# Kernel tuning notes

Hardware: AMD Instinct MI355X
Metric: run time of the kernel (lower is better)

## Reference

```python
import jax, jax.numpy as jnp
import numpy as np

T, B, E, H = 1024, 8, 1024, 16
HD = E // H                       # 64
SCALE = float(HD * 1) ** -0.5     # scaling_factor = 1


def setup_inputs() -> dict:
    key = jax.random.key(0)
    ks = jax.random.split(key, 7)
    s = 0.02
    return {
        "query": jax.random.normal(ks[0], (T, B, E), jnp.float32),
        "key_padding_mask": jax.random.bernoulli(ks[1], 0.1, (B, T)),
        "attn_bias": jax.random.normal(ks[2], (1, H, T, T), jnp.float32) * 0.1,
        "wq": jax.random.normal(ks[3], (1, E, E), jnp.float32) * s,
        "wk": jax.random.normal(ks[4], (1, E, E), jnp.float32) * s,
        "wv": jax.random.normal(ks[5], (1, E, E), jnp.float32) * s,
        "wo": jax.random.normal(ks[6], (1, E, E), jnp.float32) * s,
    }


def _group_linear(x, w):
    # x: (T, B, nb*din), w: (nb, din, dout) -> (T, B, nb*dout). nb=1 here.
    t, b, _ = x.shape
    nb, din, dout = w.shape
    y = jnp.einsum('xnd,nde->xne', x.reshape(t * b, nb, din), w)
    return y.reshape(t, b, nb * dout)


def reference(query, key_padding_mask, attn_bias, wq, wk, wv, wo):
    q = _group_linear(query, wq) * SCALE
    k = _group_linear(query, wk)
    v = _group_linear(query, wv)

    # (T, B, E) -> (B*H, T, HD), matching torch view+transpose
    def split_heads(x):
        return x.reshape(T, B * H, HD).transpose(1, 0, 2)

    q, k, v = split_heads(q), split_heads(k), split_heads(v)

    scores = jnp.einsum('bth,bsh->bts', q, k).reshape(B, H, T, T)
    scores = scores + attn_bias
    scores = jnp.where(key_padding_mask[:, None, None, :], -jnp.inf, scores)
    probs = jax.nn.softmax(scores.astype(jnp.float32), axis=-1).astype(query.dtype)

    vh = v.reshape(B, H, T, HD)  # (B*H,T,HD) -> (B,H,S,HD)
    attn = jnp.einsum('bhts,bhsd->tbhd', probs, vh).reshape(T, B, H * HD)
    return _group_linear(attn, wo)
```

## Files before the change

kernel.cpp:

```cpp
#include <hip/hip_runtime.h>


typedef __bf16 bf16x8 __attribute__((ext_vector_type(8)));
typedef float f32x4 __attribute__((ext_vector_type(4)));

#define LOG2E 1.4426950408889634f
#define QSCALE 0.18033688011112042f

static __device__ __forceinline__ unsigned short f2bf_rn(float f) {
  union { float f; unsigned u; } x;
  x.f = f;
  unsigned r = (x.u + 0x7fffu + ((x.u >> 16) & 1u)) >> 16;
  return (unsigned short)r;
}
static __device__ __forceinline__ unsigned short f2bf(float f) {
  union { float f; unsigned u; } x;
  x.f = f;
  return (unsigned short)((x.u + 0x8000u) >> 16);
}

static __device__ __forceinline__ void async_cp16(const void* g, void* l) {
  __builtin_amdgcn_global_load_lds((__attribute__((address_space(1))) void*)g,
                                   (__attribute__((address_space(3))) void*)l,
                                   16, 0, 0);
}

__global__ void k_cvt(const float* __restrict__ src, unsigned short* __restrict__ dst) {
  const int idx = blockIdx.x * 256 + threadIdx.x;
  const float4 f = ((const float4*)src)[idx];
  unsigned lo = (unsigned)f2bf_rn(f.x) | ((unsigned)f2bf_rn(f.y) << 16);
  unsigned hi = (unsigned)f2bf_rn(f.z) | ((unsigned)f2bf_rn(f.w) << 16);
  uint2 v; v.x = lo; v.y = hi;
  *(uint2*)(dst + (size_t)idx * 4) = v;
}

__global__ void k_mask(const int* __restrict__ mask, float* __restrict__ Mfg) {
  const int i = blockIdx.x * 256 + threadIdx.x;
  Mfg[i] = mask[i] ? -1e30f : 0.f;
}

__global__ void k_transw(const float* __restrict__ src, unsigned short* __restrict__ dst) {
  __shared__ float tile[32][33];
  const int bx = blockIdx.x << 5;
  const int by = blockIdx.y << 5;
  const int tx = threadIdx.x, ty = threadIdx.y;
#pragma unroll
  for (int i = 0; i < 32; i += 8)
    tile[ty + i][tx] = src[(size_t)(by + ty + i) * 1024 + bx + tx];
  __syncthreads();
#pragma unroll
  for (int i = 0; i < 32; i += 8)
    dst[(size_t)(bx + ty + i) * 1024 + by + tx] = f2bf_rn(tile[tx][ty + i]);
}

__global__ __launch_bounds__(256, 2) void k_biasT(const float* __restrict__ bias,
                                                  unsigned short* __restrict__ B2) {
  __shared__ unsigned short tile[128 * 132];
  const int tid = threadIdx.x;
  const int ss = blockIdx.x, tt = blockIdx.y, h = blockIdx.z;
  const float* src = bias + ((long)h * 1024 + tt * 128) * 1024 + ss * 128;
#pragma unroll
  for (int c = 0; c < 16; ++c) {
    int flat = c * 256 + tid;
    int row = flat >> 5, col = (flat & 31) << 2;
    float4 v = *(const float4*)(src + (long)row * 1024 + col);
    unsigned short* t4 = &tile[row * 132 + col];
    t4[0] = f2bf_rn(v.x * LOG2E); t4[1] = f2bf_rn(v.y * LOG2E);
    t4[2] = f2bf_rn(v.z * LOG2E); t4[3] = f2bf_rn(v.w * LOG2E);
  }
  __syncthreads();
  const int wid = tid >> 6, lane = tid & 63, lanelo = lane & 15, quad = lane >> 4;
  unsigned short outv[64];
#pragma unroll
  for (int mi = 0; mi < 2; ++mi)
#pragma unroll
    for (int nj = 0; nj < 8; ++nj)
#pragma unroll
      for (int r = 0; r < 4; ++r)
        outv[mi * 32 + nj * 4 + r] =
            tile[(wid * 32 + mi * 16 + quad * 4 + r) * 132 + nj * 16 + lanelo];
  unsigned short* dst = B2 + ((((long)(h * 8 + tt) * 8 + ss) * 256 + tid) << 6);
#pragma unroll
  for (int i = 0; i < 8; ++i) ((uint4*)dst)[i] = ((const uint4*)outv)[i];
}

static __device__ __forceinline__ void gemm_tile_128x128(
    const unsigned short* __restrict__ A, const unsigned short* __restrict__ Bt,
    int K, long m0, long n0,
    unsigned short* As, unsigned short* Bs, f32x4 acc[4][4]) {
  const int tid = threadIdx.x;
  const int wid = tid >> 6;
  const int lane = tid & 63;
  const int lanelo = lane & 15;
  const int quad = lane >> 4;
  const int wm = (wid >> 1) << 6;
  const int wn = (wid & 1) << 6;
  const int srow = tid >> 2;
  const int scol = (tid & 3) << 3;

  for (int k0 = 0; k0 < K; k0 += 32) {
    __syncthreads();
    {
      const unsigned short* ga0 = A + (m0 + srow) * K + k0 + scol;
      const unsigned short* ga1 = A + (m0 + srow + 64) * K + k0 + scol;
      const unsigned short* gb0 = Bt + (n0 + srow) * K + k0 + scol;
      const unsigned short* gb1 = Bt + (n0 + srow + 64) * K + k0 + scol;
      char* la = (char*)As + wid * 1024;
      char* lb = (char*)Bs + wid * 1024;
      async_cp16(ga0, la);
      async_cp16(ga1, la + 4096);
      async_cp16(gb0, lb);
      async_cp16(gb1, lb + 4096);
    }
    __syncthreads();
    bf16x8 a[4], b[4];
#pragma unroll
    for (int i = 0; i < 4; ++i) {
      a[i] = *(const bf16x8*)(As + (wm + i * 16 + lanelo) * 32 + quad * 8);
      b[i] = *(const bf16x8*)(Bs + (wn + i * 16 + lanelo) * 32 + quad * 8);
    }
#pragma unroll
    for (int i = 0; i < 4; ++i)
#pragma unroll
      for (int j = 0; j < 4; ++j)
        acc[i][j] = __builtin_amdgcn_mfma_f32_16x16x32_bf16(a[i], b[j], acc[i][j], 0, 0, 0);
  }
}

__global__ __launch_bounds__(256, 2) void k_gemm_qkv(
    const unsigned short* __restrict__ A, const unsigned short* __restrict__ Bt,
    unsigned short* __restrict__ Qh, unsigned short* __restrict__ Kh,
    unsigned short* __restrict__ Vt) {
  __shared__ unsigned short smem[9216];
  unsigned short* As = smem;
  unsigned short* Bs = smem + 4096;
  f32x4 acc[4][4];
  const f32x4 z4 = {0.f, 0.f, 0.f, 0.f};
#pragma unroll
  for (int i = 0; i < 4; ++i)
#pragma unroll
    for (int j = 0; j < 4; ++j) acc[i][j] = z4;

  const long m0 = (long)blockIdx.y * 128;
  const long n0 = (long)blockIdx.x * 128;
  gemm_tile_128x128(A, Bt, 1024, m0, n0, As, Bs, acc);

  const int tid = threadIdx.x;
  const int wid = tid >> 6;
  const int lane = tid & 63;
  const int lanelo = lane & 15;
  const int quad = lane >> 4;
  const int wm = (wid >> 1) << 6;
  const int wn = (wid & 1) << 6;
  const int which = (int)(blockIdx.x >> 3);

  if (which == 2) {
    unsigned short* Vt_s = smem;
    const long t0g = m0 >> 3;
#pragma unroll
    for (int half = 0; half < 2; ++half) {
      __syncthreads();
      if ((wid & 1) == half) {
#pragma unroll
        for (int mi = 0; mi < 4; ++mi)
#pragma unroll
          for (int nj = 0; nj < 4; ++nj)
#pragma unroll
            for (int r = 0; r < 4; ++r)
              Vt_s[(wm + mi * 16 + quad * 4 + r) * 72 + nj * 16 + lanelo] =
                  f2bf(acc[mi][nj][r]);
      }
      __syncthreads();
      const int h = (((int)(n0 & 1023)) >> 6) + half;
#pragma unroll
      for (int pp = 0; pp < 2; ++pp) {
        int p = tid + pp * 256;
        int b = p >> 6, d = p & 63;
        long off = ((long)(b * 16 + h)) << 16;
        __attribute__((aligned(16))) unsigned short vals[16];
#pragma unroll
        for (int t = 0; t < 16; ++t) vals[t] = Vt_s[(t * 8 + b) * 72 + d];
        uint4* dst = (uint4*)(Vt + off + (long)d * 1024 + t0g);
        dst[0] = ((const uint4*)vals)[0];
        dst[1] = ((const uint4*)vals)[1];
      }
    }
  } else {
#pragma unroll
    for (int mi = 0; mi < 4; ++mi)
#pragma unroll
      for (int nj = 0; nj < 4; ++nj)
#pragma unroll
        for (int r = 0; r < 4; ++r) {
          int m = (int)m0 + wm + mi * 16 + quad * 4 + r;
          int n = (int)n0 + wn + nj * 16 + lanelo;
          float v = acc[mi][nj][r];
          int t = m >> 3, b = m & 7;
          int e = n & 1023, h = e >> 6, d = e & 63;
          long off = ((long)(b * 16 + h)) << 16;
          if (which == 0)
            Qh[off + t * 64 + d] = f2bf(v * QSCALE);
          else
            Kh[off + t * 64 + d] = f2bf(v);
        }
  }
}

__global__ __launch_bounds__(512, 4) void k_attn(
    const unsigned short* __restrict__ Qh, const unsigned short* __restrict__ Kh,
    const unsigned short* __restrict__ Vt, const unsigned short* __restrict__ B2,
    const float* __restrict__ Mfg, unsigned short* __restrict__ A2) {
  __shared__ unsigned short Ks[128 * 72];
  __shared__ unsigned short Vs[64 * 136];
  __shared__ unsigned short Ps[128 * 72];

  const int tid = threadIdx.x;
  const int wid = tid >> 6;
  const int lane = tid & 63;
  const int lanelo = lane & 15;
  const int quad = lane >> 4;
  const int bh = blockIdx.x;
  const int b = bh >> 4, h = bh & 15;
  const int tt = blockIdx.y;
  const int t0 = tt * 128;
  const long head = (long)bh << 16;

  bf16x8 aq[2];
#pragma unroll
  for (int ks = 0; ks < 2; ++ks)
    aq[ks] = *(const bf16x8*)(Qh + head +
                              (long)(t0 + wid * 16 + lanelo) * 64 +
                              ks * 32 + quad * 8);

  const f32x4 z4 = {0.f, 0.f, 0.f, 0.f};
  f32x4 Oacc[4];
#pragma unroll
  for (int dj = 0; dj < 4; ++dj) Oacc[dj] = z4;
  float mrow[4], lrow[4];
#pragma unroll
  for (int r = 0; r < 4; ++r) { mrow[r] = -1e30f; lrow[r] = 0.f; }

  const long biasbase = (((long)(h * 8 + tt) * 8) * 256 + (wid >> 1) * 64 + lane) * 64 +
                        (wid & 1) * 32;

  for (int s0 = 0; s0 < 1024; s0 += 128) {
    bf16x8 bfr[4];
    {
      const bf16x8* bp8 = (const bf16x8*)(B2 + biasbase + ((long)(s0 >> 7) * 256 << 6));
#pragma unroll
      for (int i = 0; i < 4; ++i) bfr[i] = bp8[i];
    }
    float madd[8];
#pragma unroll
    for (int nj = 0; nj < 8; ++nj)
      madd[nj] = Mfg[(long)b * 1024 + s0 + nj * 16 + lanelo];

    __syncthreads();
#pragma unroll
    for (int c = 0; c < 2; ++c) {
      int flat = c * 4096 + tid * 8;
      int row = flat >> 6, col = flat & 63;
      uint4 v = *(const uint4*)(Kh + head + (long)(s0 + row) * 64 + col);
      *(uint4*)&Ks[row * 72 + col] = v;
    }
#pragma unroll
    for (int c = 0; c < 2; ++c) {
      int flat = c * 4096 + tid * 8;
      int row = flat >> 7, col = flat & 127;
      uint4 v = *(const uint4*)(Vt + head + (long)row * 1024 + s0 + col);
      *(uint4*)&Vs[row * 136 + col] = v;
    }
    __syncthreads();

    f32x4 S[8];
#pragma unroll
    for (int nj = 0; nj < 8; ++nj)
#pragma unroll
      for (int r = 0; r < 4; ++r)
        S[nj][r] = (float)bfr[nj >> 1][(nj & 1) * 4 + r] + madd[nj];

#pragma unroll
    for (int ks = 0; ks < 2; ++ks) {
      bf16x8 bk[8];
#pragma unroll
      for (int nj = 0; nj < 8; ++nj)
        bk[nj] = *(const bf16x8*)(Ks + (nj * 16 + lanelo) * 72 + ks * 32 + quad * 8);
#pragma unroll
      for (int nj = 0; nj < 8; ++nj)
        S[nj] = __builtin_amdgcn_mfma_f32_16x16x32_bf16(aq[ks], bk[nj], S[nj], 0, 0, 0);
    }

#pragma unroll
    for (int r = 0; r < 4; ++r) {
      float mx = S[0][r];
#pragma unroll
      for (int nj = 1; nj < 8; ++nj) mx = fmaxf(mx, S[nj][r]);
      mx = fmaxf(mx, __shfl_xor(mx, 1, 16));
      mx = fmaxf(mx, __shfl_xor(mx, 2, 16));
      mx = fmaxf(mx, __shfl_xor(mx, 4, 16));
      mx = fmaxf(mx, __shfl_xor(mx, 8, 16));
      float mold = mrow[r];
      float mnew = fmaxf(mold, mx);
      float al = exp2f(mold - mnew);
      mrow[r] = mnew;
      float rs = 0.f;
#pragma unroll
      for (int nj = 0; nj < 8; ++nj) {
        float p = exp2f(S[nj][r] - mnew);
        S[nj][r] = p;
        rs += p;
      }
      rs += __shfl_xor(rs, 1, 16);
      rs += __shfl_xor(rs, 2, 16);
      rs += __shfl_xor(rs, 4, 16);
      rs += __shfl_xor(rs, 8, 16);
      lrow[r] = lrow[r] * al + rs;
#pragma unroll
      for (int dj = 0; dj < 4; ++dj) Oacc[dj][r] *= al;
    }

#pragma unroll
    for (int half = 0; half < 2; ++half) {
#pragma unroll
      for (int njl = 0; njl < 4; ++njl)
#pragma unroll
        for (int r = 0; r < 4; ++r)
          Ps[(wid * 16 + quad * 4 + r) * 72 + njl * 16 + lanelo] =
              f2bf(S[half * 4 + njl][r]);
#pragma unroll
      for (int ks2 = 0; ks2 < 2; ++ks2) {
        const int ks = half * 2 + ks2;
        bf16x8 ap, bv[4];
        ap = *(const bf16x8*)(Ps + (wid * 16 + lanelo) * 72 + ks2 * 32 + quad * 8);
#pragma unroll
        for (int dj = 0; dj < 4; ++dj)
          bv[dj] = *(const bf16x8*)(Vs + (dj * 16 + lanelo) * 136 + ks * 32 + quad * 8);
#pragma unroll
        for (int dj = 0; dj < 4; ++dj)
          Oacc[dj] = __builtin_amdgcn_mfma_f32_16x16x32_bf16(ap, bv[dj], Oacc[dj], 0, 0, 0);
      }
    }
  }

#pragma unroll
  for (int r = 0; r < 4; ++r) {
    float rinv = __builtin_amdgcn_rcpf(lrow[r]);
    int t = t0 + wid * 16 + quad * 4 + r;
#pragma unroll
    for (int dj = 0; dj < 4; ++dj) {
      int d = dj * 16 + lanelo;
      A2[(long)(t * 8 + b) * 1024 + h * 64 + d] = f2bf(Oacc[dj][r] * rinv);
    }
  }
}

__global__ __launch_bounds__(256, 2) void k_gemm_out(
    const unsigned short* __restrict__ A, const unsigned short* __restrict__ Bt,
    float* __restrict__ out) {
  __shared__ unsigned short As[128 * 32];
  __shared__ unsigned short Bs[128 * 32];
  f32x4 acc[4][4];
  const f32x4 z4 = {0.f, 0.f, 0.f, 0.f};
#pragma unroll
  for (int i = 0; i < 4; ++i)
#pragma unroll
    for (int j = 0; j < 4; ++j) acc[i][j] = z4;

  const long m0 = (long)blockIdx.y * 128;
  const long n0 = (long)blockIdx.x * 128;
  gemm_tile_128x128(A, Bt, 1024, m0, n0, As, Bs, acc);

  const int tid = threadIdx.x;
  const int wid = tid >> 6;
  const int lane = tid & 63;
  const int lanelo = lane & 15;
  const int quad = lane >> 4;
  const int wm = (wid >> 1) << 6;
  const int wn = (wid & 1) << 6;
#pragma unroll
  for (int mi = 0; mi < 4; ++mi)
#pragma unroll
    for (int nj = 0; nj < 4; ++nj)
#pragma unroll
      for (int r = 0; r < 4; ++r) {
        long m = m0 + wm + mi * 16 + quad * 4 + r;
        long n = n0 + wn + nj * 16 + lanelo;
        out[m * 1024 + n] = acc[mi][nj][r];
      }
}

extern "C" void kernel_launch(void* const* d_in, const int* in_sizes, int n_in,
                              void* d_out, int out_size, void* d_ws, size_t ws_size,
                              hipStream_t stream) {
  const float* query = (const float*)d_in[0];
  const int* mask = (const int*)d_in[1];
  const float* bias = (const float*)d_in[2];
  const float* wq = (const float*)d_in[3];
  const float* wk = (const float*)d_in[4];
  const float* wv = (const float*)d_in[5];
  const float* wo = (const float*)d_in[6];
  float* out = (float*)d_out;

  char* ws = (char*)d_ws;
  const size_t MB = 1024 * 1024;
  unsigned short* Abuf  = (unsigned short*)(ws);
  unsigned short* WqkvT = (unsigned short*)(ws + 16 * MB);
  unsigned short* WoT   = (unsigned short*)(ws + 22 * MB);
  unsigned short* Qh    = (unsigned short*)(ws + 24 * MB);
  unsigned short* Kh    = (unsigned short*)(ws + 40 * MB);
  unsigned short* Vt    = (unsigned short*)(ws + 56 * MB);
  unsigned short* A2    = (unsigned short*)(ws + 72 * MB);
  unsigned short* B2    = (unsigned short*)(ws + 88 * MB);
  float*          Mfg   = (float*)(ws + 120 * MB);

  k_cvt<<<dim3(8192), dim3(256), 0, stream>>>(query, Abuf);
  k_mask<<<dim3(32), dim3(256), 0, stream>>>(mask, Mfg);
  dim3 tb(32, 8);
  k_transw<<<dim3(32, 32), tb, 0, stream>>>(wq, WqkvT);
  k_transw<<<dim3(32, 32), tb, 0, stream>>>(wk, WqkvT + 1024 * 1024);
  k_transw<<<dim3(32, 32), tb, 0, stream>>>(wv, WqkvT + 2 * 1024 * 1024);
  k_transw<<<dim3(32, 32), tb, 0, stream>>>(wo, WoT);
  k_biasT<<<dim3(8, 8, 16), dim3(256), 0, stream>>>(bias, B2);
  k_gemm_qkv<<<dim3(24, 64), dim3(256), 0, stream>>>(Abuf, WqkvT, Qh, Kh, Vt);
  k_attn<<<dim3(128, 8), dim3(512), 0, stream>>>(Qh, Kh, Vt, B2, Mfg, A2);
  k_gemm_out<<<dim3(8, 64), dim3(256), 0, stream>>>(A2, WoT, out);
}
```

Baseline: 381.8 us.

## Prefetch next K/V tile and bias into registers during attention compute

Software-pipelines the flash-attention loop. The next iteration's K and V tiles are loaded into registers and stored to LDS at the top of the following iteration, and the next bias and mask values are fetched right after the QK MFMAs. The goal is to hide global memory latency behind compute instead of stalling at each tile load. In exchange, register use goes up, which could lower occupancy.

```diff
diff --git a/kernel.cpp b/kernel.cpp
--- a/kernel.cpp
+++ b/kernel.cpp
@@ -225,6 +225,13 @@
   const int t0 = tt * 128;
   const long head = (long)bh << 16;
 
+  const int krow = tid >> 3, kcol = (tid & 7) << 3;
+  const int vrow = tid >> 4, vcol = (tid & 15) << 3;
+  const unsigned short* kg = Kh + head + (long)krow * 64 + kcol;
+  const unsigned short* vg = Vt + head + (long)vrow * 1024 + vcol;
+  unsigned short* kl = &Ks[krow * 72 + kcol];
+  unsigned short* vl = &Vs[vrow * 136 + vcol];
+
   bf16x8 aq[2];
 #pragma unroll
   for (int ks = 0; ks < 2; ++ks)
@@ -243,32 +250,34 @@
   const long biasbase = (((long)(h * 8 + tt) * 8) * 256 + (wid >> 1) * 64 + lane) * 64 +
                         (wid & 1) * 32;
 
+  uint4 kreg[2], vreg[2];
+  kreg[0] = *(const uint4*)(kg);
+  kreg[1] = *(const uint4*)(kg + 64 * 64);
+  vreg[0] = *(const uint4*)(vg);
+  vreg[1] = *(const uint4*)(vg + 32 * 1024);
+  bf16x8 bfr[4];
+  {
+    const bf16x8* bp8 = (const bf16x8*)(B2 + biasbase);
+#pragma unroll
+    for (int i = 0; i < 4; ++i) bfr[i] = bp8[i];
+  }
+  float madd[8];
+#pragma unroll
+  for (int nj = 0; nj < 8; ++nj)
+    madd[nj] = Mfg[(long)b * 1024 + nj * 16 + lanelo];
+
   for (int s0 = 0; s0 < 1024; s0 += 128) {
-    bf16x8 bfr[4];
-    {
-      const bf16x8* bp8 = (const bf16x8*)(B2 + biasbase + ((long)(s0 >> 7) * 256 << 6));
-#pragma unroll
-      for (int i = 0; i < 4; ++i) bfr[i] = bp8[i];
-    }
-    float madd[8];
-#pragma unroll
-    for (int nj = 0; nj < 8; ++nj)
-      madd[nj] = Mfg[(long)b * 1024 + s0 + nj * 16 + lanelo];
-
     __syncthreads();
-#pragma unroll
-    for (int c = 0; c < 2; ++c) {
-      int flat = c * 4096 + tid * 8;
-      int row = flat >> 6, col = flat & 63;
-      uint4 v = *(const uint4*)(Kh + head + (long)(s0 + row) * 64 + col);
-      *(uint4*)&Ks[row * 72 + col] = v;
-    }
-#pragma unroll
-    for (int c = 0; c < 2; ++c) {
-      int flat = c * 4096 + tid * 8;
-      int row = flat >> 7, col = flat & 127;
-      uint4 v = *(const uint4*)(Vt + head + (long)row * 1024 + s0 + col);
-      *(uint4*)&Vs[row * 136 + col] = v;
+    *(uint4*)kl = kreg[0];
+    *(uint4*)(kl + 64 * 72) = kreg[1];
+    *(uint4*)vl = vreg[0];
+    *(uint4*)(vl + 32 * 136) = vreg[1];
+    if (s0 < 896) {
+      const long s1 = s0 + 128;
+      kreg[0] = *(const uint4*)(kg + s1 * 64);
+      kreg[1] = *(const uint4*)(kg + s1 * 64 + 64 * 64);
+      vreg[0] = *(const uint4*)(vg + s1);
+      vreg[1] = *(const uint4*)(vg + s1 + 32 * 1024);
     }
     __syncthreads();
 
@@ -288,6 +297,15 @@
 #pragma unroll
       for (int nj = 0; nj < 8; ++nj)
         S[nj] = __builtin_amdgcn_mfma_f32_16x16x32_bf16(aq[ks], bk[nj], S[nj], 0, 0, 0);
+    }
+
+    if (s0 < 896) {
+      const bf16x8* bp8 = (const bf16x8*)(B2 + biasbase + ((long)((s0 >> 7) + 1) * 256 << 6));
+#pragma unroll
+      for (int i = 0; i < 4; ++i) bfr[i] = bp8[i];
+#pragma unroll
+      for (int nj = 0; nj < 8; ++nj)
+        madd[nj] = Mfg[(long)b * 1024 + s0 + 128 + nj * 16 + lanelo];
     }
 
 #pragma unroll
```

New measurement: 420.9 us. 10.2% more time.

## Double-buffer K tiles with async global-to-LDS loads and XOR-swizzled layouts

Applied to the files above, without the earlier changes.

Replaces the synchronous register-staged K/V tile loads in the attention kernel with global_load_lds async copies. K is double-buffered so the next tile is prefetched during the current QK^T and softmax, and V is loaded asynchronously in parallel with the score computation. Padded LDS strides are replaced by XOR swizzles, and the P staging buffer reuses the current K buffer, shrinking shared memory. This aims to hide global load latency and reduce LDS footprint, at the cost of hand-placed vmcnt waits and barriers that must match the outstanding-load count exactly.

```diff
diff --git a/kernel.cpp b/kernel.cpp
--- a/kernel.cpp
+++ b/kernel.cpp
@@ -210,9 +210,8 @@
     const unsigned short* __restrict__ Qh, const unsigned short* __restrict__ Kh,
     const unsigned short* __restrict__ Vt, const unsigned short* __restrict__ B2,
     const float* __restrict__ Mfg, unsigned short* __restrict__ A2) {
-  __shared__ unsigned short Ks[128 * 72];
-  __shared__ unsigned short Vs[64 * 136];
-  __shared__ unsigned short Ps[128 * 72];
+  __shared__ unsigned short smem[24576];
+  unsigned short* Vs = smem + 16384;
 
   const int tid = threadIdx.x;
   const int wid = tid >> 6;
@@ -225,6 +224,16 @@
   const int t0 = tt * 128;
   const long head = (long)bh << 16;
 
+  const int krow0 = wid * 8 + (lane >> 3);
+  const int ksw = (((lane & 7) ^ (lane >> 3)) << 3);
+  const unsigned short* kg = Kh + head + (long)krow0 * 64 + ksw;
+  const int vrow = wid * 4 + (lane >> 4);
+  const int vsw = (((lane & 15) ^ (vrow & 15)) << 3);
+  const unsigned short* vg = Vt + head + (long)vrow * 1024 + vsw;
+
+  async_cp16(kg, (char*)smem + (wid << 10));
+  async_cp16(kg + 64 * 64, (char*)smem + (wid << 10) + 8192);
+
   bf16x8 aq[2];
 #pragma unroll
   for (int ks = 0; ks < 2; ++ks)
@@ -243,10 +252,18 @@
   const long biasbase = (((long)(h * 8 + tt) * 8) * 256 + (wid >> 1) * 64 + lane) * 64 +
                         (wid & 1) * 32;
 
-  for (int s0 = 0; s0 < 1024; s0 += 128) {
+  for (int it = 0; it < 8; ++it) {
+    const int s0 = it << 7;
+    unsigned short* Kcur = smem + ((it & 1) << 13);
+    unsigned short* Kalt = smem + (((it + 1) & 1) << 13);
+
+    asm volatile("s_waitcnt vmcnt(0)" ::: "memory");
+    __builtin_amdgcn_s_barrier();
+    __builtin_amdgcn_sched_barrier(0);
+
     bf16x8 bfr[4];
     {
-      const bf16x8* bp8 = (const bf16x8*)(B2 + biasbase + ((long)(s0 >> 7) * 256 << 6));
+      const bf16x8* bp8 = (const bf16x8*)(B2 + biasbase + ((long)it * 256 << 6));
 #pragma unroll
       for (int i = 0; i < 4; ++i) bfr[i] = bp8[i];
     }
@@ -255,22 +272,13 @@
     for (int nj = 0; nj < 8; ++nj)
       madd[nj] = Mfg[(long)b * 1024 + s0 + nj * 16 + lanelo];
 
-    __syncthreads();
-#pragma unroll
-    for (int c = 0; c < 2; ++c) {
-      int flat = c * 4096 + tid * 8;
-      int row = flat >> 6, col = flat & 63;
-      uint4 v = *(const uint4*)(Kh + head + (long)(s0 + row) * 64 + col);
-      *(uint4*)&Ks[row * 72 + col] = v;
-    }
-#pragma unroll
-    for (int c = 0; c < 2; ++c) {
-      int flat = c * 4096 + tid * 8;
-      int row = flat >> 7, col = flat & 127;
-      uint4 v = *(const uint4*)(Vt + head + (long)row * 1024 + s0 + col);
-      *(uint4*)&Vs[row * 136 + col] = v;
-    }
-    __syncthreads();
+    async_cp16(vg + s0, (char*)Vs + (wid << 10));
+    async_cp16(vg + 32 * 1024 + s0, (char*)Vs + (wid << 10) + 8192);
+    if (it < 7) {
+      const unsigned short* kgs = kg + (long)(s0 + 128) * 64;
+      async_cp16(kgs, (char*)Kalt + (wid << 10));
+      async_cp16(kgs + 64 * 64, (char*)Kalt + (wid << 10) + 8192);
+    }
 
     f32x4 S[8];
 #pragma unroll
@@ -284,7 +292,8 @@
       bf16x8 bk[8];
 #pragma unroll
       for (int nj = 0; nj < 8; ++nj)
-        bk[nj] = *(const bf16x8*)(Ks + (nj * 16 + lanelo) * 72 + ks * 32 + quad * 8);
+        bk[nj] = *(const bf16x8*)(Kcur + (nj * 16 + lanelo) * 64 +
+                                  (((ks * 4 + quad) ^ (lanelo & 7)) << 3));
 #pragma unroll
       for (int nj = 0; nj < 8; ++nj)
         S[nj] = __builtin_amdgcn_mfma_f32_16x16x32_bf16(aq[ks], bk[nj], S[nj], 0, 0, 0);
@@ -319,22 +328,33 @@
       for (int dj = 0; dj < 4; ++dj) Oacc[dj][r] *= al;
     }
 
+    if (it < 7) asm volatile("s_waitcnt vmcnt(2)" ::: "memory");
+    else        asm volatile("s_waitcnt vmcnt(0)" ::: "memory");
+    __builtin_amdgcn_s_barrier();
+    __builtin_amdgcn_sched_barrier(0);
+
+    unsigned short* Ps = Kcur;
 #pragma unroll
     for (int half = 0; half < 2; ++half) {
 #pragma unroll
       for (int njl = 0; njl < 4; ++njl)
 #pragma unroll
-        for (int r = 0; r < 4; ++r)
-          Ps[(wid * 16 + quad * 4 + r) * 72 + njl * 16 + lanelo] =
+        for (int r = 0; r < 4; ++r) {
+          const int rw7 = ((quad << 2) + r) & 7;
+          Ps[(wid * 16 + (quad << 2) + r) * 64 +
+             ((((njl << 1) + (lanelo >> 3)) ^ rw7) << 3) + (lanelo & 7)] =
               f2bf(S[half * 4 + njl][r]);
+        }
 #pragma unroll
       for (int ks2 = 0; ks2 < 2; ++ks2) {
         const int ks = half * 2 + ks2;
         bf16x8 ap, bv[4];
-        ap = *(const bf16x8*)(Ps + (wid * 16 + lanelo) * 72 + ks2 * 32 + quad * 8);
+        ap = *(const bf16x8*)(Ps + (wid * 16 + lanelo) * 64 +
+                              (((ks2 * 4 + quad) ^ (lanelo & 7)) << 3));
 #pragma unroll
         for (int dj = 0; dj < 4; ++dj)
-          bv[dj] = *(const bf16x8*)(Vs + (dj * 16 + lanelo) * 136 + ks * 32 + quad * 8);
+          bv[dj] = *(const bf16x8*)(Vs + (dj * 16 + lanelo) * 128 +
+                                    (((ks * 4 + quad) ^ lanelo) << 3));
 #pragma unroll
         for (int dj = 0; dj < 4; ++dj)
           Oacc[dj] = __builtin_amdgcn_mfma_f32_16x16x32_bf16(ap, bv[dj], Oacc[dj], 0, 0, 0);
```

After: 383.6 us. Within noise of the previous version (+0.5%).
